# Kernel optimization log

Measured on AMD Instinct MI355X. Metric: run time of the kernel, lower is better.

The kernel has to match this reference:

```python
import jax, jax.numpy as jnp
import numpy as np

N = 100000
E = 1600000
D_IN = 128
D_OUT = 128
NEG_SLOPE = 0.01  # PyTorch LeakyReLU default


def setup_inputs() -> dict:
    key = jax.random.key(0)
    ks = jax.random.split(key, 6)
    x = jax.random.normal(ks[0], (N, D_IN), dtype=jnp.float32)
    src = jax.random.randint(ks[1], (E,), 0, N, dtype=jnp.int32)
    dst = jax.random.randint(ks[2], (E,), 0, N, dtype=jnp.int32)
    e_attn = jax.random.uniform(ks[3], (E,), dtype=jnp.float32)
    # Xavier-normal-ish init for linear weights
    std = float(np.sqrt(2.0 / (D_IN + D_OUT)))
    W1 = jax.random.normal(ks[4], (D_OUT, D_IN), dtype=jnp.float32) * std
    W2 = jax.random.normal(ks[5], (D_OUT, D_IN), dtype=jnp.float32) * std
    b1 = jnp.zeros((D_OUT,), dtype=jnp.float32)
    b2 = jnp.zeros((D_OUT,), dtype=jnp.float32)
    return {"x": x, "src": src, "dst": dst, "e_attn": e_attn,
            "W1": W1, "b1": b1, "W2": W2, "b2": b2}


def leaky_relu(v):
    return jnp.where(v >= 0, v, NEG_SLOPE * v)


def reference(x, src, dst, e_attn, W1, b1, W2, b2):
    # Edge-weighted gather-scatter: h_n[d] = sum_{e: dst(e)=d} a_e * x[src(e)]
    msgs = x[src] * e_attn[:, None]                      # [E, D_IN]
    h_n = jax.ops.segment_sum(msgs, dst, num_segments=N)  # [N, D_IN]
    # Bi-interaction: LeakyReLU(W1(x + h_n)) + LeakyReLU(W2(x * h_n))
    add_part = leaky_relu(jnp.einsum('nd,od->no', x + h_n, W1) + b1)
    mul_part = leaky_relu(jnp.einsum('nd,od->no', x * h_n, W2) + b2)
    return add_part + mul_part  # dropout p=0.0 -> identity
```

## Files before the change

### kernel.cpp

```cpp
#include <hip/hip_runtime.h>

#define N_NODES 100000
#define E_EDGES 1600000
#define D 128
#define AP 132
#define ASTR 136

typedef short s16x8 __attribute__((ext_vector_type(8)));
typedef unsigned short u16x8 __attribute__((ext_vector_type(8)));
typedef float f32x4 __attribute__((ext_vector_type(4)));

__device__ __forceinline__ unsigned short f2bf(float f) {
    union { float f; unsigned u; } v;
    v.f = f;
    unsigned r = v.u + 0x7FFFu + ((v.u >> 16) & 1u);
    return (unsigned short)(r >> 16);
}

__device__ __forceinline__ float bf2f(unsigned short u) {
    union { unsigned u; float f; } v;
    v.u = ((unsigned)u) << 16;
    return v.f;
}

__device__ __forceinline__ float lrelu(float v) {
    return v >= 0.0f ? v : 0.01f * v;
}

__global__ __launch_bounds__(256) void prep_kernel(
    const int* __restrict__ dst, int* __restrict__ cnt,
    unsigned char* __restrict__ rank, int stride,
    const float* __restrict__ x, unsigned short* __restrict__ xbf, int do_xconv,
    const float* __restrict__ W1, const float* __restrict__ W2,
    unsigned short* __restrict__ Wswz) {
    int b = blockIdx.x;
    int t = threadIdx.x;
    if (b < 6250) {
        int e = b * 256 + t;
        rank[e] = (unsigned char)atomicAdd(&cnt[(size_t)dst[e] * stride], 1);
    } else if (b < 12500) {
        if (!do_xconv) return;
        int idx = (b - 6250) * 256 + t;
        const float4* xp = (const float4*)(x) + (size_t)idx * 2;
        float4 a = xp[0], bb = xp[1];
        u16x8 o;
        o[0] = f2bf(a.x);  o[1] = f2bf(a.y);  o[2] = f2bf(a.z);  o[3] = f2bf(a.w);
        o[4] = f2bf(bb.x); o[5] = f2bf(bb.y); o[6] = f2bf(bb.z); o[7] = f2bf(bb.w);
        ((u16x8*)(xbf))[idx] = o;
    } else {
        int tid = (b - 12500) * 256 + t;
        if (tid >= 2 * 4 * 8 * 64) return;
        int lane = tid & 63;
        int ct   = (tid >> 6) & 7;
        int ks   = (tid >> 9) & 3;
        int mat  = tid >> 11;
        const float* W = mat ? W2 : W1;
        int o  = ct * 16 + (lane & 15);
        int k0 = ks * 32 + (lane >> 4) * 8;
        const float* sp = W + (size_t)o * D + k0;
        u16x8 w;
#pragma unroll
        for (int j = 0; j < 8; ++j) w[j] = f2bf(sp[j]);
        ((u16x8*)(Wswz))[tid] = w;
    }
}

__global__ __launch_bounds__(256) void alloc_kernel(
    const int* __restrict__ cnt, int stride, int* __restrict__ cursor,
    int2* __restrict__ begend, int n) {
    int gid = blockIdx.x * 256 + threadIdx.x;
    int lane = threadIdx.x & 63;
    int c = (gid < n) ? cnt[(size_t)gid * stride] : 0;
    int incl = c;
#pragma unroll
    for (int ofs = 1; ofs < 64; ofs <<= 1) {
        int tt = __shfl_up(incl, ofs);
        if (lane >= ofs) incl += tt;
    }
    int tot = __shfl(incl, 63);
    int base = 0;
    if (lane == 63) base = atomicAdd(cursor, tot);
    base = __shfl(base, 63);
    int beg = base + incl - c;
    if (gid < n) begend[gid] = make_int2(beg, beg + c);
}

__global__ __launch_bounds__(256) void fillC_kernel(
    const int* __restrict__ src, const int* __restrict__ dst,
    const float* __restrict__ ea, const int2* __restrict__ begend,
    const unsigned char* __restrict__ rank, int2* __restrict__ csr) {
    int gid = blockIdx.x * 256 + threadIdx.x;
    int d = dst[gid];
    int pos = begend[d].x + (int)rank[gid];
    csr[pos] = make_int2(src[gid], __float_as_int(ea[gid]));
}

__global__ __launch_bounds__(512, 8) void fused_gg_kernel(
    const unsigned short* __restrict__ xbf, const int2* __restrict__ csr,
    const int2* __restrict__ begend,
    const unsigned short* __restrict__ Wswz,
    const float* __restrict__ b1, const float* __restrict__ b2,
    float* __restrict__ out) {
    __shared__ unsigned short A[2][64 * ASTR];

    const int n0 = blockIdx.x * 64;
    const int t = threadIdx.x;
    const int lane = t & 63;
    const int wv = t >> 6;
    const int q = lane >> 4;
    const int li = lane & 15;

    for (int j = 0; j < 8; ++j) {
        const int row = wv * 8 + j;
        const int node = n0 + row;
        int beg = 0, end = 0;
        if (node < N_NODES) {
            int2 be = begend[node];
            beg = be.x;
            end = be.y;
        }

        float a0[8], a1[8];
#pragma unroll
        for (int d = 0; d < 8; ++d) { a0[d] = 0.f; a1[d] = 0.f; }

        int i = beg + q;
        for (; i + 4 < end; i += 8) {
            int2 p0 = csr[i];
            int2 p1 = csr[i + 4];
            float w0 = __int_as_float(p0.y);
            float w1 = __int_as_float(p1.y);
            u16x8 v0 = ((const u16x8*)(xbf + (size_t)p0.x * D))[li];
            u16x8 v1 = ((const u16x8*)(xbf + (size_t)p1.x * D))[li];
#pragma unroll
            for (int d = 0; d < 8; ++d) {
                a0[d] += w0 * bf2f(v0[d]);
                a1[d] += w1 * bf2f(v1[d]);
            }
        }
        if (i < end) {
            int2 p0 = csr[i];
            float w0 = __int_as_float(p0.y);
            u16x8 v0 = ((const u16x8*)(xbf + (size_t)p0.x * D))[li];
#pragma unroll
            for (int d = 0; d < 8; ++d) a0[d] += w0 * bf2f(v0[d]);
        }
#pragma unroll
        for (int d = 0; d < 8; ++d) a0[d] += a1[d];
#pragma unroll
        for (int d = 0; d < 8; ++d) a0[d] += __shfl_xor(a0[d], 16);
#pragma unroll
        for (int d = 0; d < 8; ++d) a0[d] += __shfl_xor(a0[d], 32);

        const int srcrow = node < N_NODES ? node : N_NODES - 1;
        if (q < 2) {
            u16x8 xu = ((const u16x8*)(xbf + (size_t)srcrow * D))[li];
            u16x8 o;
#pragma unroll
            for (int dd = 0; dd < 8; ++dd) {
                float xv = bf2f(xu[dd]);
                o[dd] = f2bf(q == 0 ? xv + a0[dd] : xv * a0[dd]);
            }
            *(u16x8*)&A[q][row * ASTR + li * 8] = o;
        }
    }

    const int ct = wv;
    float bb1 = b1[ct * 16 + li];
    float bb2 = b2[ct * 16 + li];
    s16x8 Bf[2][4];
#pragma unroll
    for (int mat = 0; mat < 2; ++mat)
#pragma unroll
        for (int ks = 0; ks < 4; ++ks)
            Bf[mat][ks] = *(const s16x8*)(
                Wswz + ((size_t)(((mat * 4 + ks) * 8 + ct) * 64 + lane)) * 8);

    __syncthreads();

    const int kq = q * 8;
#pragma unroll
    for (int mt = 0; mt < 4; ++mt) {
        f32x4 acc0 = (f32x4){0.f, 0.f, 0.f, 0.f};
        f32x4 acc1 = (f32x4){0.f, 0.f, 0.f, 0.f};

        const int arow = mt * 16 + li;
#pragma unroll
        for (int ks = 0; ks < 4; ++ks) {
            s16x8 aa0 = *(const s16x8*)&A[0][arow * ASTR + ks * 32 + kq];
            s16x8 aa1 = *(const s16x8*)&A[1][arow * ASTR + ks * 32 + kq];
            acc0 = __builtin_amdgcn_mfma_f32_16x16x32_bf16(aa0, Bf[0][ks], acc0, 0, 0, 0);
            acc1 = __builtin_amdgcn_mfma_f32_16x16x32_bf16(aa1, Bf[1][ks], acc1, 0, 0, 0);
        }

        const int oc = ct * 16 + li;
#pragma unroll
        for (int r = 0; r < 4; ++r) {
            int node = n0 + mt * 16 + q * 4 + r;
            if (node < N_NODES) {
                float v = lrelu(acc0[r] + bb1) + lrelu(acc1[r] + bb2);
                out[(size_t)node * D + oc] = v;
            }
        }
    }
}

__global__ __launch_bounds__(256) void gather_f32_kernel(
    const float* __restrict__ x, const int2* __restrict__ csr,
    const int2* __restrict__ begend, float* __restrict__ h) {
    int node = blockIdx.x * 4 + (threadIdx.x >> 6);
    int lane = threadIdx.x & 63;
    int2 be = begend[node];
    int beg = be.x;
    int end = be.y;
    float2 acc0 = make_float2(0.f, 0.f);
    float2 acc1 = make_float2(0.f, 0.f);
    int e = beg;
    for (; e + 1 < end; e += 2) {
        int2 p0 = csr[e];
        int2 p1 = csr[e + 1];
        float a0 = __int_as_float(p0.y);
        float a1 = __int_as_float(p1.y);
        float2 v0 = ((const float2*)(x + (size_t)p0.x * D))[lane];
        float2 v1 = ((const float2*)(x + (size_t)p1.x * D))[lane];
        acc0.x += a0 * v0.x; acc0.y += a0 * v0.y;
        acc1.x += a1 * v1.x; acc1.y += a1 * v1.y;
    }
    if (e < end) {
        int2 p0 = csr[e];
        float a0 = __int_as_float(p0.y);
        float2 v0 = ((const float2*)(x + (size_t)p0.x * D))[lane];
        acc0.x += a0 * v0.x; acc0.y += a0 * v0.y;
    }
    acc0.x += acc1.x; acc0.y += acc1.y;
    ((float2*)(h + (size_t)node * D))[lane] = acc0;
}

__global__ __launch_bounds__(256, 4) void mfma_gemm_t1_kernel(
    const float* __restrict__ xf, const float* __restrict__ h,
    const unsigned short* __restrict__ Wswz,
    const float* __restrict__ b1, const float* __restrict__ b2,
    float* __restrict__ out) {
    __shared__ unsigned short A[2][64 * ASTR];
    const int n0 = blockIdx.x * 64;
    const int t = threadIdx.x;
    const int lane = t & 63;
    const int wv = t >> 6;
#pragma unroll
    for (int i = 0; i < 8; ++i) {
        int s = t + i * 256;
        int row = s >> 5;
        int c4 = s & 31;
        int srcrow = n0 + row;
        if (srcrow >= N_NODES) srcrow = N_NODES - 1;
        float4 xv = ((const float4*)(xf + (size_t)srcrow * D))[c4];
        float4 hv = ((const float4*)(h + (size_t)srcrow * D))[c4];
        ushort4 av, mv;
        av.x = f2bf(xv.x + hv.x); av.y = f2bf(xv.y + hv.y);
        av.z = f2bf(xv.z + hv.z); av.w = f2bf(xv.w + hv.w);
        mv.x = f2bf(xv.x * hv.x); mv.y = f2bf(xv.y * hv.y);
        mv.z = f2bf(xv.z * hv.z); mv.w = f2bf(xv.w * hv.w);
        *(ushort4*)&A[0][row * ASTR + c4 * 4] = av;
        *(ushort4*)&A[1][row * ASTR + c4 * 4] = mv;
    }
    s16x8 Bf[2][2][4];
    float bb1[2], bb2[2];
#pragma unroll
    for (int ci = 0; ci < 2; ++ci) {
        int ct = wv + ci * 4;
        bb1[ci] = b1[ct * 16 + (lane & 15)];
        bb2[ci] = b2[ct * 16 + (lane & 15)];
#pragma unroll
        for (int mat = 0; mat < 2; ++mat)
#pragma unroll
            for (int ks = 0; ks < 4; ++ks)
                Bf[ci][mat][ks] = *(const s16x8*)(
                    Wswz + ((size_t)(((mat * 4 + ks) * 8 + ct) * 64 + lane)) * 8);
    }
    __syncthreads();
    const int quad = lane >> 4;
    const int kq = quad * 8;
#pragma unroll
    for (int mt = 0; mt < 4; ++mt) {
        f32x4 acc[2][2];
#pragma unroll
        for (int ci = 0; ci < 2; ++ci)
#pragma unroll
            for (int p = 0; p < 2; ++p) acc[ci][p] = (f32x4){0.f, 0.f, 0.f, 0.f};
        const int arow = mt * 16 + (lane & 15);
#pragma unroll
        for (int ks = 0; ks < 4; ++ks) {
            s16x8 aa0 = *(const s16x8*)&A[0][arow * ASTR + ks * 32 + kq];
            s16x8 aa1 = *(const s16x8*)&A[1][arow * ASTR + ks * 32 + kq];
#pragma unroll
            for (int ci = 0; ci < 2; ++ci) {
                acc[ci][0] = __builtin_amdgcn_mfma_f32_16x16x32_bf16(
                    aa0, Bf[ci][0][ks], acc[ci][0], 0, 0, 0);
                acc[ci][1] = __builtin_amdgcn_mfma_f32_16x16x32_bf16(
                    aa1, Bf[ci][1][ks], acc[ci][1], 0, 0, 0);
            }
        }
#pragma unroll
        for (int ci = 0; ci < 2; ++ci) {
            int oc = (wv + ci * 4) * 16 + (lane & 15);
#pragma unroll
            for (int r = 0; r < 4; ++r) {
                int node = n0 + mt * 16 + quad * 4 + r;
                if (node < N_NODES) {
                    float v = lrelu(acc[ci][0][r] + bb1[ci])
                            + lrelu(acc[ci][1][r] + bb2[ci]);
                    out[(size_t)node * D + oc] = v;
                }
            }
        }
    }
}

__global__ __launch_bounds__(256) void scatter_kernel(
    const float* __restrict__ x, const int* __restrict__ src,
    const int* __restrict__ dst, const float* __restrict__ ea,
    float* __restrict__ h, int E) {
    int idx = blockIdx.x * 256 + threadIdx.x;
    int e = idx >> 5;
    int lane = idx & 31;
    if (e >= E) return;
    int s = src[e];
    int d = dst[e];
    float a = ea[e];
    float4 v = ((const float4*)(x + (size_t)s * D))[lane];
    float* hp = h + (size_t)d * D + lane * 4;
    atomicAdd(hp + 0, a * v.x);
    atomicAdd(hp + 1, a * v.y);
    atomicAdd(hp + 2, a * v.z);
    atomicAdd(hp + 3, a * v.w);
}

__global__ __launch_bounds__(256) void gemm_kernel(
    const float* __restrict__ x, const float* __restrict__ h,
    const float* __restrict__ W1, const float* __restrict__ b1,
    const float* __restrict__ W2, const float* __restrict__ b2,
    float* __restrict__ out) {
    __shared__ float Aadd[32 * AP];
    __shared__ float Amul[32 * AP];
    const int n0 = blockIdx.x * 32;
    const int t = threadIdx.x;
#pragma unroll
    for (int i = 0; i < 4; ++i) {
        int fi = t + i * 256;
        int row = fi >> 5;
        int c4 = fi & 31;
        float4 xv = ((const float4*)(x + (size_t)(n0 + row) * D))[c4];
        float4 hv = ((const float4*)(h + (size_t)(n0 + row) * D))[c4];
        float4 av = make_float4(xv.x + hv.x, xv.y + hv.y, xv.z + hv.z, xv.w + hv.w);
        float4 mv = make_float4(xv.x * hv.x, xv.y * hv.y, xv.z * hv.z, xv.w * hv.w);
        *((float4*)&Aadd[row * AP + c4 * 4]) = av;
        *((float4*)&Amul[row * AP + c4 * 4]) = mv;
    }
    __syncthreads();
    const int m0 = (t >> 5) * 4;
    const int o0 = (t & 31) * 4;
    float acc1[4][4];
    float acc2[4][4];
#pragma unroll
    for (int i = 0; i < 4; ++i)
#pragma unroll
        for (int j = 0; j < 4; ++j) { acc1[i][j] = 0.0f; acc2[i][j] = 0.0f; }
#pragma unroll 4
    for (int d = 0; d < D; d += 4) {
        float4 a[4], m[4], w1[4], w2[4];
#pragma unroll
        for (int i = 0; i < 4; ++i) a[i] = *(const float4*)&Aadd[(m0 + i) * AP + d];
#pragma unroll
        for (int i = 0; i < 4; ++i) m[i] = *(const float4*)&Amul[(m0 + i) * AP + d];
#pragma unroll
        for (int j = 0; j < 4; ++j) w1[j] = *(const float4*)&W1[(size_t)(o0 + j) * D + d];
#pragma unroll
        for (int j = 0; j < 4; ++j) w2[j] = *(const float4*)&W2[(size_t)(o0 + j) * D + d];
#pragma unroll
        for (int i = 0; i < 4; ++i)
#pragma unroll
            for (int j = 0; j < 4; ++j) {
                acc1[i][j] += a[i].x * w1[j].x + a[i].y * w1[j].y
                            + a[i].z * w1[j].z + a[i].w * w1[j].w;
                acc2[i][j] += m[i].x * w2[j].x + m[i].y * w2[j].y
                            + m[i].z * w2[j].z + m[i].w * w2[j].w;
            }
    }
#pragma unroll
    for (int i = 0; i < 4; ++i) {
        float4 r;
        float v1, v2;
        v1 = lrelu(acc1[i][0] + b1[o0 + 0]); v2 = lrelu(acc2[i][0] + b2[o0 + 0]); r.x = v1 + v2;
        v1 = lrelu(acc1[i][1] + b1[o0 + 1]); v2 = lrelu(acc2[i][1] + b2[o0 + 1]); r.y = v1 + v2;
        v1 = lrelu(acc1[i][2] + b1[o0 + 2]); v2 = lrelu(acc2[i][2] + b2[o0 + 2]); r.z = v1 + v2;
        v1 = lrelu(acc1[i][3] + b1[o0 + 3]); v2 = lrelu(acc2[i][3] + b2[o0 + 3]); r.w = v1 + v2;
        ((float4*)(out + (size_t)(n0 + m0 + i) * D))[t & 31] = r;
    }
}

extern "C" void kernel_launch(void* const* d_in, const int* in_sizes, int n_in,
                              void* d_out, int out_size, void* d_ws, size_t ws_size,
                              hipStream_t stream) {
    const float* x   = (const float*)d_in[0];
    const int*   src = (const int*)d_in[1];
    const int*   dst = (const int*)d_in[2];
    const float* ea  = (const float*)d_in[3];
    const float* W1  = (const float*)d_in[4];
    const float* b1  = (const float*)d_in[5];
    const float* W2  = (const float*)d_in[6];
    const float* b2  = (const float*)d_in[7];
    float* out = (float*)d_out;
    char* ws = (char*)d_ws;

    auto align256 = [](size_t v) { return (v + 255) & ~(size_t)255; };

    const size_t SZ_WSWZ = 2 * 4 * 8 * 64 * 8 * sizeof(unsigned short);
    const size_t SZ_BE   = (size_t)N_NODES * sizeof(int2);
    const size_t SZ_RANK = (size_t)E_EDGES;
    const size_t SZ_CSR  = (size_t)E_EDGES * sizeof(int2);
    const size_t SZ_XBF  = (size_t)N_NODES * D * sizeof(unsigned short);

    const int NB_E = 6250;
    const int NB_N = (N_NODES + 255) / 256;
    const int GB   = (N_NODES + 63) / 64;

    auto try_top = [&](int stride) -> bool {
        size_t sz_cnt = (size_t)N_NODES * stride * sizeof(int);
        size_t o_cnt  = align256(SZ_WSWZ);
        size_t o_cur  = o_cnt + align256(sz_cnt);
        size_t o_be   = o_cur + 256;
        size_t o_rank = o_be + align256(SZ_BE);
        size_t o_csr  = o_rank + align256(SZ_RANK);
        size_t o_xbf  = o_csr + align256(SZ_CSR);
        size_t need   = o_xbf + align256(SZ_XBF);
        if (ws_size < need) return false;
        unsigned short* Wswz = (unsigned short*)ws;
        int*  cnt  = (int*)(ws + o_cnt);
        int*  cur  = (int*)(ws + o_cur);
        int2* be   = (int2*)(ws + o_be);
        unsigned char* rank = (unsigned char*)(ws + o_rank);
        int2* csr  = (int2*)(ws + o_csr);
        unsigned short* xbf = (unsigned short*)(ws + o_xbf);
        hipMemsetAsync(cnt, 0, align256(sz_cnt) + 256, stream);
        prep_kernel<<<12516, 256, 0, stream>>>(dst, cnt, rank, stride,
                                               x, xbf, 1, W1, W2, Wswz);
        alloc_kernel<<<NB_N, 256, 0, stream>>>(cnt, stride, cur, be, N_NODES);
        fillC_kernel<<<NB_E, 256, 0, stream>>>(src, dst, ea, be, rank, csr);
        fused_gg_kernel<<<GB, 512, 0, stream>>>(xbf, csr, be, Wswz, b1, b2, out);
        return true;
    };
    if (try_top(16)) return;
    if (try_top(1)) return;

    {
        size_t sz_cnt = (size_t)N_NODES * sizeof(int);
        size_t o_cnt  = align256(SZ_WSWZ);
        size_t o_cur  = o_cnt + align256(sz_cnt);
        size_t o_be   = o_cur + 256;
        size_t o_rank = o_be + align256(SZ_BE);
        size_t o_csr  = o_rank + align256(SZ_RANK);
        size_t need   = o_csr + align256(SZ_CSR);
        if (ws_size >= need) {
            unsigned short* Wswz = (unsigned short*)ws;
            int*  cnt  = (int*)(ws + o_cnt);
            int*  cur  = (int*)(ws + o_cur);
            int2* be   = (int2*)(ws + o_be);
            unsigned char* rank = (unsigned char*)(ws + o_rank);
            int2* csr  = (int2*)(ws + o_csr);
            hipMemsetAsync(cnt, 0, align256(sz_cnt) + 256, stream);
            prep_kernel<<<12516, 256, 0, stream>>>(dst, cnt, rank, 1,
                                                   x, nullptr, 0, W1, W2, Wswz);
            alloc_kernel<<<NB_N, 256, 0, stream>>>(cnt, 1, cur, be, N_NODES);
            fillC_kernel<<<NB_E, 256, 0, stream>>>(src, dst, ea, be, rank, csr);
            float* h = out;
            gather_f32_kernel<<<N_NODES / 4, 256, 0, stream>>>(x, csr, be, h);
            mfma_gemm_t1_kernel<<<GB, 256, 0, stream>>>(x, h, Wswz, b1, b2, out);
            return;
        }
    }

    {
        float* h = out;
        hipMemsetAsync(h, 0, (size_t)N_NODES * D * sizeof(float), stream);
        int total = E_EDGES * 32;
        scatter_kernel<<<(total + 255) / 256, 256, 0, stream>>>(x, src, dst, ea,
                                                                h, E_EDGES);
        gemm_kernel<<<N_NODES / 32, 256, 0, stream>>>(x, h, W1, b1, W2, b2, out);
    }
}
```

Measured before the change: 319.6 us.

## Fuse CSR build and gather-GEMM into one cooperative persistent kernel

```diff
diff --git a/kernel.cpp b/kernel.cpp
--- a/kernel.cpp
+++ b/kernel.cpp
@@ -1,10 +1,14 @@
 #include <hip/hip_runtime.h>
+#include <hip/hip_cooperative_groups.h>
+
+namespace cg = cooperative_groups;
 
 #define N_NODES 100000
 #define E_EDGES 1600000
 #define D 128
 #define AP 132
 #define ASTR 136
+#define NPAD64 100032
 
 typedef short s16x8 __attribute__((ext_vector_type(8)));
 typedef unsigned short u16x8 __attribute__((ext_vector_type(8)));
@@ -25,6 +29,179 @@
 
 __device__ __forceinline__ float lrelu(float v) {
     return v >= 0.0f ? v : 0.01f * v;
+}
+
+__global__ __launch_bounds__(512, 8) void mega_kernel(
+    const float* __restrict__ x, const int* __restrict__ src,
+    const int* __restrict__ dst, const float* __restrict__ ea,
+    const float* __restrict__ W1, const float* __restrict__ b1,
+    const float* __restrict__ W2, const float* __restrict__ b2,
+    int* __restrict__ cnt, int* __restrict__ cursor, int2* __restrict__ begend,
+    unsigned char* __restrict__ rank, int2* __restrict__ csr,
+    unsigned short* __restrict__ xbf, unsigned short* __restrict__ Wswz,
+    float* __restrict__ out) {
+    cg::grid_group gg = cg::this_grid();
+    const int t = threadIdx.x;
+    const int gsz = gridDim.x * 512;
+    const int gtid = blockIdx.x * 512 + t;
+    const int lane = t & 63;
+    const int wv = t >> 6;
+
+    for (int i = gtid; i < N_NODES * 16; i += gsz) cnt[i] = 0;
+    if (gtid == 0) *cursor = 0;
+    __threadfence();
+    gg.sync();
+
+    for (int e = gtid; e < E_EDGES; e += gsz)
+        rank[e] = (unsigned char)atomicAdd(&cnt[(size_t)dst[e] * 16], 1);
+    for (int idx = gtid; idx < N_NODES * D / 8; idx += gsz) {
+        const float4* xp = (const float4*)(x) + (size_t)idx * 2;
+        float4 a = xp[0], b = xp[1];
+        u16x8 o;
+        o[0] = f2bf(a.x); o[1] = f2bf(a.y); o[2] = f2bf(a.z); o[3] = f2bf(a.w);
+        o[4] = f2bf(b.x); o[5] = f2bf(b.y); o[6] = f2bf(b.z); o[7] = f2bf(b.w);
+        ((u16x8*)(xbf))[idx] = o;
+    }
+    for (int tid = gtid; tid < 2 * 4 * 8 * 64; tid += gsz) {
+        int wl  = tid & 63;
+        int ct  = (tid >> 6) & 7;
+        int ks  = (tid >> 9) & 3;
+        int mat = tid >> 11;
+        const float* W = mat ? W2 : W1;
+        int o  = ct * 16 + (wl & 15);
+        int k0 = ks * 32 + (wl >> 4) * 8;
+        const float* sp = W + (size_t)o * D + k0;
+        u16x8 w;
+#pragma unroll
+        for (int j = 0; j < 8; ++j) w[j] = f2bf(sp[j]);
+        ((u16x8*)(Wswz))[tid] = w;
+    }
+    __threadfence();
+    gg.sync();
+
+    for (int gid = gtid; gid < NPAD64; gid += gsz) {
+        int c = (gid < N_NODES) ? cnt[(size_t)gid * 16] : 0;
+        int incl = c;
+#pragma unroll
+        for (int ofs = 1; ofs < 64; ofs <<= 1) {
+            int tt = __shfl_up(incl, ofs);
+            if (lane >= ofs) incl += tt;
+        }
+        int tot = __shfl(incl, 63);
+        int base = 0;
+        if (lane == 63) base = atomicAdd(cursor, tot);
+        base = __shfl(base, 63);
+        int beg = base + incl - c;
+        if (gid < N_NODES) begend[gid] = make_int2(beg, beg + c);
+    }
+    __threadfence();
+    gg.sync();
+
+    for (int e = gtid; e < E_EDGES; e += gsz) {
+        int d = dst[e];
+        int pos = begend[d].x + (int)rank[e];
+        csr[pos] = make_int2(src[e], __float_as_int(ea[e]));
+    }
+    __threadfence();
+    gg.sync();
+
+    __shared__ unsigned short A[2][64 * ASTR];
+    const int q = lane >> 4;
+    const int li = lane & 15;
+    const int ct = wv;
+    const float bb1 = b1[ct * 16 + li];
+    const float bb2 = b2[ct * 16 + li];
+    s16x8 Bf[2][4];
+#pragma unroll
+    for (int mat = 0; mat < 2; ++mat)
+#pragma unroll
+        for (int ks = 0; ks < 4; ++ks)
+            Bf[mat][ks] = *(const s16x8*)(
+                Wswz + ((size_t)(((mat * 4 + ks) * 8 + ct) * 64 + lane)) * 8);
+    const int kq = q * 8;
+    const int ntiles = (N_NODES + 63) / 64;
+
+    for (int tile = blockIdx.x; tile < ntiles; tile += gridDim.x) {
+        const int n0 = tile * 64;
+        __syncthreads();
+
+        for (int j = 0; j < 8; ++j) {
+            const int row = wv * 8 + j;
+            const int node = n0 + row;
+            int beg = 0, end = 0;
+            if (node < N_NODES) {
+                int2 be = begend[node];
+                beg = be.x;
+                end = be.y;
+            }
+            float a0[8], a1[8];
+#pragma unroll
+            for (int d = 0; d < 8; ++d) { a0[d] = 0.f; a1[d] = 0.f; }
+            int i = beg + q;
+            for (; i + 4 < end; i += 8) {
+                int2 p0 = csr[i];
+                int2 p1 = csr[i + 4];
+                float w0 = __int_as_float(p0.y);
+                float w1 = __int_as_float(p1.y);
+                u16x8 v0 = ((const u16x8*)(xbf + (size_t)p0.x * D))[li];
+                u16x8 v1 = ((const u16x8*)(xbf + (size_t)p1.x * D))[li];
+#pragma unroll
+                for (int d = 0; d < 8; ++d) {
+                    a0[d] += w0 * bf2f(v0[d]);
+                    a1[d] += w1 * bf2f(v1[d]);
+                }
+            }
+            if (i < end) {
+                int2 p0 = csr[i];
+                float w0 = __int_as_float(p0.y);
+                u16x8 v0 = ((const u16x8*)(xbf + (size_t)p0.x * D))[li];
+#pragma unroll
+                for (int d = 0; d < 8; ++d) a0[d] += w0 * bf2f(v0[d]);
+            }
+#pragma unroll
+            for (int d = 0; d < 8; ++d) a0[d] += a1[d];
+#pragma unroll
+            for (int d = 0; d < 8; ++d) a0[d] += __shfl_xor(a0[d], 16);
+#pragma unroll
+            for (int d = 0; d < 8; ++d) a0[d] += __shfl_xor(a0[d], 32);
+
+            const int srcrow = node < N_NODES ? node : N_NODES - 1;
+            if (q < 2) {
+                u16x8 xu = ((const u16x8*)(xbf + (size_t)srcrow * D))[li];
+                u16x8 o;
+#pragma unroll
+                for (int dd = 0; dd < 8; ++dd) {
+                    float xv = bf2f(xu[dd]);
+                    o[dd] = f2bf(q == 0 ? xv + a0[dd] : xv * a0[dd]);
+                }
+                *(u16x8*)&A[q][row * ASTR + li * 8] = o;
+            }
+        }
+        __syncthreads();
+
+#pragma unroll
+        for (int mt = 0; mt < 4; ++mt) {
+            f32x4 acc0 = (f32x4){0.f, 0.f, 0.f, 0.f};
+            f32x4 acc1 = (f32x4){0.f, 0.f, 0.f, 0.f};
+            const int arow = mt * 16 + li;
+#pragma unroll
+            for (int ks = 0; ks < 4; ++ks) {
+                s16x8 aa0 = *(const s16x8*)&A[0][arow * ASTR + ks * 32 + kq];
+                s16x8 aa1 = *(const s16x8*)&A[1][arow * ASTR + ks * 32 + kq];
+                acc0 = __builtin_amdgcn_mfma_f32_16x16x32_bf16(aa0, Bf[0][ks], acc0, 0, 0, 0);
+                acc1 = __builtin_amdgcn_mfma_f32_16x16x32_bf16(aa1, Bf[1][ks], acc1, 0, 0, 0);
+            }
+            const int oc = ct * 16 + li;
+#pragma unroll
+            for (int r = 0; r < 4; ++r) {
+                int node = n0 + mt * 16 + q * 4 + r;
+                if (node < N_NODES) {
+                    float v = lrelu(acc0[r] + bb1) + lrelu(acc1[r] + bb2);
+                    out[(size_t)node * D + oc] = v;
+                }
+            }
+        }
+    }
 }
 
 __global__ __launch_bounds__(256) void prep_kernel(
@@ -119,11 +296,9 @@
             beg = be.x;
             end = be.y;
         }
-
         float a0[8], a1[8];
 #pragma unroll
         for (int d = 0; d < 8; ++d) { a0[d] = 0.f; a1[d] = 0.f; }
-
         int i = beg + q;
         for (; i + 4 < end; i += 8) {
             int2 p0 = csr[i];
@@ -183,7 +358,6 @@
     for (int mt = 0; mt < 4; ++mt) {
         f32x4 acc0 = (f32x4){0.f, 0.f, 0.f, 0.f};
         f32x4 acc1 = (f32x4){0.f, 0.f, 0.f, 0.f};
-
         const int arow = mt * 16 + li;
 #pragma unroll
         for (int ks = 0; ks < 4; ++ks) {
@@ -192,7 +366,6 @@
             acc0 = __builtin_amdgcn_mfma_f32_16x16x32_bf16(aa0, Bf[0][ks], acc0, 0, 0, 0);
             acc1 = __builtin_amdgcn_mfma_f32_16x16x32_bf16(aa1, Bf[1][ks], acc1, 0, 0, 0);
         }
-
         const int oc = ct * 16 + li;
 #pragma unroll
         for (int r = 0; r < 4; ++r) {
@@ -424,23 +597,68 @@
     const int NB_N = (N_NODES + 255) / 256;
     const int GB   = (N_NODES + 63) / 64;
 
+    size_t sz_cnt16 = (size_t)N_NODES * 16 * sizeof(int);
+    size_t o_cnt  = align256(SZ_WSWZ);
+    size_t o_cur  = o_cnt + align256(sz_cnt16);
+    size_t o_be   = o_cur + 256;
+    size_t o_rank = o_be + align256(SZ_BE);
+    size_t o_csr  = o_rank + align256(SZ_RANK);
+    size_t o_xbf  = o_csr + align256(SZ_CSR);
+    size_t need16 = o_xbf + align256(SZ_XBF);
+
+    if (ws_size >= need16) {
+        static int coop_grid = -2;
+        if (coop_grid == -2) {
+            int dev = 0;
+            hipGetDevice(&dev);
+            int coop = 0;
+            hipDeviceGetAttribute(&coop, hipDeviceAttributeCooperativeLaunch, dev);
+            int nb = 0;
+            hipError_t e1 = hipOccupancyMaxActiveBlocksPerMultiprocessor(
+                &nb, reinterpret_cast<const void*>(mega_kernel), 512, 0);
+            hipDeviceProp_t prop;
+            hipError_t e2 = hipGetDeviceProperties(&prop, dev);
+            coop_grid = (coop && e1 == hipSuccess && e2 == hipSuccess && nb > 0)
+                        ? nb * prop.multiProcessorCount : -1;
+        }
+        if (coop_grid > 0) {
+            unsigned short* Wswz = (unsigned short*)ws;
+            int*  cnt  = (int*)(ws + o_cnt);
+            int*  cur  = (int*)(ws + o_cur);
+            int2* be   = (int2*)(ws + o_be);
+            unsigned char* rank = (unsigned char*)(ws + o_rank);
+            int2* csr  = (int2*)(ws + o_csr);
+            unsigned short* xbf = (unsigned short*)(ws + o_xbf);
+            void* args[] = {
+                (void*)&x, (void*)&src, (void*)&dst, (void*)&ea,
+                (void*)&W1, (void*)&b1, (void*)&W2, (void*)&b2,
+                (void*)&cnt, (void*)&cur, (void*)&be, (void*)&rank,
+                (void*)&csr, (void*)&xbf, (void*)&Wswz, (void*)&out};
+            hipError_t err = hipLaunchCooperativeKernel(
+                reinterpret_cast<const void*>(mega_kernel),
+                dim3(coop_grid), dim3(512), args, 0, stream);
+            if (err == hipSuccess) return;
+            coop_grid = -1;
+        }
+    }
+
     auto try_top = [&](int stride) -> bool {
         size_t sz_cnt = (size_t)N_NODES * stride * sizeof(int);
-        size_t o_cnt  = align256(SZ_WSWZ);
-        size_t o_cur  = o_cnt + align256(sz_cnt);
-        size_t o_be   = o_cur + 256;
-        size_t o_rank = o_be + align256(SZ_BE);
-        size_t o_csr  = o_rank + align256(SZ_RANK);
-        size_t o_xbf  = o_csr + align256(SZ_CSR);
-        size_t need   = o_xbf + align256(SZ_XBF);
+        size_t p_cnt  = align256(SZ_WSWZ);
+        size_t p_cur  = p_cnt + align256(sz_cnt);
+        size_t p_be   = p_cur + 256;
+        size_t p_rank = p_be + align256(SZ_BE);
+        size_t p_csr  = p_rank + align256(SZ_RANK);
+        size_t p_xbf  = p_csr + align256(SZ_CSR);
+        size_t need   = p_xbf + align256(SZ_XBF);
         if (ws_size < need) return false;
         unsigned short* Wswz = (unsigned short*)ws;
-        int*  cnt  = (int*)(ws + o_cnt);
-        int*  cur  = (int*)(ws + o_cur);
-        int2* be   = (int2*)(ws + o_be);
-        unsigned char* rank = (unsigned char*)(ws + o_rank);
-        int2* csr  = (int2*)(ws + o_csr);
-        unsigned short* xbf = (unsigned short*)(ws + o_xbf);
+        int*  cnt  = (int*)(ws + p_cnt);
+        int*  cur  = (int*)(ws + p_cur);
+        int2* be   = (int2*)(ws + p_be);
+        unsigned char* rank = (unsigned char*)(ws + p_rank);
+        int2* csr  = (int2*)(ws + p_csr);
+        unsigned short* xbf = (unsigned short*)(ws + p_xbf);
         hipMemsetAsync(cnt, 0, align256(sz_cnt) + 256, stream);
         prep_kernel<<<12516, 256, 0, stream>>>(dst, cnt, rank, stride,
                                                x, xbf, 1, W1, W2, Wswz);
@@ -454,19 +672,19 @@
 
     {
         size_t sz_cnt = (size_t)N_NODES * sizeof(int);
-        size_t o_cnt  = align256(SZ_WSWZ);
-        size_t o_cur  = o_cnt + align256(sz_cnt);
-        size_t o_be   = o_cur + 256;
-        size_t o_rank = o_be + align256(SZ_BE);
-        size_t o_csr  = o_rank + align256(SZ_RANK);
-        size_t need   = o_csr + align256(SZ_CSR);
+        size_t p_cnt  = align256(SZ_WSWZ);
+        size_t p_cur  = p_cnt + align256(sz_cnt);
+        size_t p_be   = p_cur + 256;
+        size_t p_rank = p_be + align256(SZ_BE);
+        size_t p_csr  = p_rank + align256(SZ_RANK);
+        size_t need   = p_csr + align256(SZ_CSR);
         if (ws_size >= need) {
             unsigned short* Wswz = (unsigned short*)ws;
-            int*  cnt  = (int*)(ws + o_cnt);
-            int*  cur  = (int*)(ws + o_cur);
-            int2* be   = (int2*)(ws + o_be);
-            unsigned char* rank = (unsigned char*)(ws + o_rank);
-            int2* csr  = (int2*)(ws + o_csr);
+            int*  cnt  = (int*)(ws + p_cnt);
+            int*  cur  = (int*)(ws + p_cur);
+            int2* be   = (int2*)(ws + p_be);
+            unsigned char* rank = (unsigned char*)(ws + p_rank);
+            int2* csr  = (int2*)(ws + p_csr);
             hipMemsetAsync(cnt, 0, align256(sz_cnt) + 256, stream);
             prep_kernel<<<12516, 256, 0, stream>>>(dst, cnt, rank, 1,
                                                    x, nullptr, 0, W1, W2, Wswz);
```

Measured after the change: 984.7 us. +208.1%, slower.
